# Performance work log

Measured on AMD Instinct MI355X. Metric: run time of the kernel, lower is better.

## Reference

```python
import jax, jax.numpy as jnp
import numpy as np

TOP_K = 8

def setup_inputs() -> dict:
    key = jax.random.key(0)
    kx, kw = jax.random.split(key)
    x = jax.random.normal(kx, (4, 8192, 2048), dtype=jnp.float32)
    # gate weight [n_routed_experts, dim]
    weight = jax.random.normal(kw, (64, 2048), dtype=jnp.float32) * 0.02
    return {"x": x, "weight": weight}

def reference(x, weight):
    # flatten tokens: [N, dim]
    xf = x.reshape(-1, x.shape[-1])
    # router logits: [N, E] = xf @ weight.T
    logits = jnp.einsum('nd,ed->ne', xf, weight)
    scores = jax.nn.softmax(logits, axis=-1)
    # top-k expert scores and indices (lax.top_k returns sorted; torch used
    # sorted=False which is an unordered set of the same elements)
    values, indices = jax.lax.top_k(scores, TOP_K)
    return values, indices
```

## Files before the change

kernel.cpp:

```cpp
#include <hip/hip_runtime.h>
#include <stdint.h>

#define DIM     2048
#define NEXP    64
#define NCHUNK  32
#define TPB     64
#define TAU     5e-5f
#define LCAP    4096

#define WFRAG_USHORTS (NCHUNK * 8192)
#define WT_OFF        (1u << 20)
#define CNT_OFF       (WT_OFF + (1u << 19))
#define LIST_OFF      (CNT_OFF + 16)

typedef __attribute__((ext_vector_type(8))) short bf16x8;
typedef __attribute__((ext_vector_type(8))) unsigned short u16x8;
typedef __attribute__((ext_vector_type(4))) float f32x4;

__device__ inline unsigned short bf16_rne(float f) {
    uint32_t u = __float_as_uint(f);
    return (unsigned short)((u + 0x7FFFu + ((u >> 16) & 1u)) >> 16);
}
__device__ inline float bf16_to_f(unsigned short h) {
    return __uint_as_float(((uint32_t)h) << 16);
}
__device__ inline uint64_t mono64(double d) {
    uint64_t u = (uint64_t)__double_as_longlong(d);
    return (u >> 63) ? ~u : (u | 0x8000000000000000ull);
}
__device__ inline double unmono64(uint64_t m) {
    uint64_t b = (m >> 63) ? (m & 0x7fffffffffffffffull) : ~m;
    return __longlong_as_double((long long)b);
}

#define SPL(F, HV, LV, J)  { unsigned short _h = bf16_rne(F); HV[J] = _h; LV[J] = bf16_rne((F) - bf16_to_f(_h)); }
#define SPLS(F, HV, LV, J) { unsigned short _h = bf16_rne(F); HV[J] = (short)_h; LV[J] = (short)bf16_rne((F) - bf16_to_f(_h)); }

__device__ __forceinline__ void g2l16(const void* g, void* l) {
    __builtin_amdgcn_global_load_lds(
        (__attribute__((address_space(1))) void*)(g),
        (__attribute__((address_space(3))) void*)(l),
        16, 0, 0);
}

__global__ __launch_bounds__(256) void wsplit_kernel(
    const float* __restrict__ wgt, unsigned short* __restrict__ wf)
{
    int g = blockIdx.x * 256 + threadIdx.x;
    int l = g & 63;
    int t = (g >> 6) & 3;
    int s = (g >> 8) & 1;
    int c = g >> 9;
    int e = (l & 15) + 16 * t;
    int k = c * 64 + s * 32 + ((l >> 4) * 8);
    const float* wp = wgt + (size_t)e * DIM + k;
    float4 f0 = *(const float4*)(wp);
    float4 f1 = *(const float4*)(wp + 4);
    u16x8 h, lo;
    SPL(f0.x, h, lo, 0) SPL(f0.y, h, lo, 1) SPL(f0.z, h, lo, 2) SPL(f0.w, h, lo, 3)
    SPL(f1.x, h, lo, 4) SPL(f1.y, h, lo, 5) SPL(f1.z, h, lo, 6) SPL(f1.w, h, lo, 7)
    size_t base = ((((size_t)(c * 2 + s) * 4 + t) * 2 + 0) * 64 + l) * 8;
    *(u16x8*)(wf + base)       = h;
    *(u16x8*)(wf + base + 512) = lo;
}

__global__ __launch_bounds__(256) void wtrans_kernel(
    const float* __restrict__ wgt, float4* __restrict__ wt, int* __restrict__ cnt)
{
    int g  = blockIdx.x * 256 + threadIdx.x;
    if (g == 0) cnt[0] = 0;
    int e  = g >> 9;
    int kq = g & 511;
    float4 v = *(const float4*)(wgt + (size_t)e * DIM + kq * 4);
    wt[(size_t)kq * 64 + e] = v;
}

#define STAGE_CHUNK(CC, XD, BD)                                                   \
    {                                                                             \
        _Pragma("unroll")                                                         \
        for (int s_ = 0; s_ < 4; ++s_) {                                          \
            int idx_ = wave * 256 + s_ * 64 + lane;                               \
            int row_ = idx_ >> 4;                                                 \
            int p_   = idx_ & 15;                                                 \
            int g_   = p_ ^ (row_ & 7);                                           \
            const unsigned char* gsrc_ = (const unsigned char*)x +                \
                (((size_t)(t0 + row_) * DIM + (CC) * 64 + g_ * 4) << 2);          \
            g2l16(gsrc_, (XD) + wave * 4096 + s_ * 1024);                         \
        }                                                                         \
        const unsigned char* wfb_ = (const unsigned char*)wf + (size_t)(CC) * 16384; \
        _Pragma("unroll")                                                         \
        for (int s_ = 0; s_ < 4; ++s_) {                                          \
            g2l16(wfb_ + wave * 4096 + s_ * 1024 + lane * 16,                     \
                  (BD) + wave * 4096 + s_ * 1024);                                \
        }                                                                         \
    }

__global__ __launch_bounds__(256) void moe_gate_mfma_kernel(
    const float* __restrict__ x, const unsigned short* __restrict__ wf,
    float* __restrict__ out, int ntok, int* __restrict__ cnt, int* __restrict__ list)
{
    __shared__ __align__(16) unsigned char smem[65536];

    const int tid  = threadIdx.x;
    const int wave = tid >> 6;
    const int lane = tid & 63;
    const int t0   = blockIdx.x * TPB;
    const int l15  = lane & 15;
    const int lg   = lane >> 4;

    unsigned char* const xb0 = smem;
    unsigned char* const xb1 = smem + 16384;
    unsigned char* const bb0 = smem + 32768;
    unsigned char* const bb1 = smem + 49152;

    f32x4 acc0 = {0.f,0.f,0.f,0.f}, acc1 = {0.f,0.f,0.f,0.f};
    f32x4 acc2 = {0.f,0.f,0.f,0.f}, acc3 = {0.f,0.f,0.f,0.f};

    STAGE_CHUNK(0, xb0, bb0);

    const int s7 = l15 & 7;
    for (int c = 0; c < NCHUNK; ++c) {
        __syncthreads();
        unsigned char* xcur = (c & 1) ? xb1 : xb0;
        unsigned char* bcur = (c & 1) ? bb1 : bb0;
        if (c + 1 < NCHUNK) {
            unsigned char* xnxt = (c & 1) ? xb0 : xb1;
            unsigned char* bnxt = (c & 1) ? bb0 : bb1;
            STAGE_CHUNK(c + 1, xnxt, bnxt);
        }

        const unsigned char* xrow = xcur + (wave * 16 + l15) * 256;
        float4 fa0 = *(const float4*)(xrow + (((2 * lg)     ^ s7) * 16));
        float4 fa1 = *(const float4*)(xrow + (((2 * lg + 1) ^ s7) * 16));
        float4 fa2 = *(const float4*)(xrow + (((8 + 2 * lg) ^ s7) * 16));
        float4 fa3 = *(const float4*)(xrow + (((9 + 2 * lg) ^ s7) * 16));

        bf16x8 Ah0, Al0, Ah1, Al1;
        SPLS(fa0.x, Ah0, Al0, 0) SPLS(fa0.y, Ah0, Al0, 1) SPLS(fa0.z, Ah0, Al0, 2) SPLS(fa0.w, Ah0, Al0, 3)
        SPLS(fa1.x, Ah0, Al0, 4) SPLS(fa1.y, Ah0, Al0, 5) SPLS(fa1.z, Ah0, Al0, 6) SPLS(fa1.w, Ah0, Al0, 7)
        SPLS(fa2.x, Ah1, Al1, 0) SPLS(fa2.y, Ah1, Al1, 1) SPLS(fa2.z, Ah1, Al1, 2) SPLS(fa2.w, Ah1, Al1, 3)
        SPLS(fa3.x, Ah1, Al1, 4) SPLS(fa3.y, Ah1, Al1, 5) SPLS(fa3.z, Ah1, Al1, 6) SPLS(fa3.w, Ah1, Al1, 7)

        const unsigned short* bu = (const unsigned short*)bcur;
        {
            bf16x8 Bh0 = *(const bf16x8*)(bu +        0 + lane * 8);
            bf16x8 Bl0 = *(const bf16x8*)(bu +      512 + lane * 8);
            bf16x8 Bh1 = *(const bf16x8*)(bu + 4096 + 0 + lane * 8);
            bf16x8 Bl1 = *(const bf16x8*)(bu + 4096 + 512 + lane * 8);
            acc0 = __builtin_amdgcn_mfma_f32_16x16x32_bf16(Ah0, Bh0, acc0, 0, 0, 0);
            acc0 = __builtin_amdgcn_mfma_f32_16x16x32_bf16(Ah0, Bl0, acc0, 0, 0, 0);
            acc0 = __builtin_amdgcn_mfma_f32_16x16x32_bf16(Al0, Bh0, acc0, 0, 0, 0);
            acc0 = __builtin_amdgcn_mfma_f32_16x16x32_bf16(Ah1, Bh1, acc0, 0, 0, 0);
            acc0 = __builtin_amdgcn_mfma_f32_16x16x32_bf16(Ah1, Bl1, acc0, 0, 0, 0);
            acc0 = __builtin_amdgcn_mfma_f32_16x16x32_bf16(Al1, Bh1, acc0, 0, 0, 0);
        }
        {
            bf16x8 Bh0 = *(const bf16x8*)(bu + 1024 + lane * 8);
            bf16x8 Bl0 = *(const bf16x8*)(bu + 1536 + lane * 8);
            bf16x8 Bh1 = *(const bf16x8*)(bu + 5120 + lane * 8);
            bf16x8 Bl1 = *(const bf16x8*)(bu + 5632 + lane * 8);
            acc1 = __builtin_amdgcn_mfma_f32_16x16x32_bf16(Ah0, Bh0, acc1, 0, 0, 0);
            acc1 = __builtin_amdgcn_mfma_f32_16x16x32_bf16(Ah0, Bl0, acc1, 0, 0, 0);
            acc1 = __builtin_amdgcn_mfma_f32_16x16x32_bf16(Al0, Bh0, acc1, 0, 0, 0);
            acc1 = __builtin_amdgcn_mfma_f32_16x16x32_bf16(Ah1, Bh1, acc1, 0, 0, 0);
            acc1 = __builtin_amdgcn_mfma_f32_16x16x32_bf16(Ah1, Bl1, acc1, 0, 0, 0);
            acc1 = __builtin_amdgcn_mfma_f32_16x16x32_bf16(Al1, Bh1, acc1, 0, 0, 0);
        }
        {
            bf16x8 Bh0 = *(const bf16x8*)(bu + 2048 + lane * 8);
            bf16x8 Bl0 = *(const bf16x8*)(bu + 2560 + lane * 8);
            bf16x8 Bh1 = *(const bf16x8*)(bu + 6144 + lane * 8);
            bf16x8 Bl1 = *(const bf16x8*)(bu + 6656 + lane * 8);
            acc2 = __builtin_amdgcn_mfma_f32_16x16x32_bf16(Ah0, Bh0, acc2, 0, 0, 0);
            acc2 = __builtin_amdgcn_mfma_f32_16x16x32_bf16(Ah0, Bl0, acc2, 0, 0, 0);
            acc2 = __builtin_amdgcn_mfma_f32_16x16x32_bf16(Al0, Bh0, acc2, 0, 0, 0);
            acc2 = __builtin_amdgcn_mfma_f32_16x16x32_bf16(Ah1, Bh1, acc2, 0, 0, 0);
            acc2 = __builtin_amdgcn_mfma_f32_16x16x32_bf16(Ah1, Bl1, acc2, 0, 0, 0);
            acc2 = __builtin_amdgcn_mfma_f32_16x16x32_bf16(Al1, Bh1, acc2, 0, 0, 0);
        }
        {
            bf16x8 Bh0 = *(const bf16x8*)(bu + 3072 + lane * 8);
            bf16x8 Bl0 = *(const bf16x8*)(bu + 3584 + lane * 8);
            bf16x8 Bh1 = *(const bf16x8*)(bu + 7168 + lane * 8);
            bf16x8 Bl1 = *(const bf16x8*)(bu + 7680 + lane * 8);
            acc3 = __builtin_amdgcn_mfma_f32_16x16x32_bf16(Ah0, Bh0, acc3, 0, 0, 0);
            acc3 = __builtin_amdgcn_mfma_f32_16x16x32_bf16(Ah0, Bl0, acc3, 0, 0, 0);
            acc3 = __builtin_amdgcn_mfma_f32_16x16x32_bf16(Al0, Bh0, acc3, 0, 0, 0);
            acc3 = __builtin_amdgcn_mfma_f32_16x16x32_bf16(Ah1, Bh1, acc3, 0, 0, 0);
            acc3 = __builtin_amdgcn_mfma_f32_16x16x32_bf16(Ah1, Bl1, acc3, 0, 0, 0);
            acc3 = __builtin_amdgcn_mfma_f32_16x16x32_bf16(Al1, Bh1, acc3, 0, 0, 0);
        }
    }

    __syncthreads();
    float* lsw = (float*)smem + wave * 1088;
    {
        const int rb = lg * 4;
        lsw[(rb + 0) * 68 +  0 + l15] = acc0[0]; lsw[(rb + 1) * 68 +  0 + l15] = acc0[1];
        lsw[(rb + 2) * 68 +  0 + l15] = acc0[2]; lsw[(rb + 3) * 68 +  0 + l15] = acc0[3];
        lsw[(rb + 0) * 68 + 16 + l15] = acc1[0]; lsw[(rb + 1) * 68 + 16 + l15] = acc1[1];
        lsw[(rb + 2) * 68 + 16 + l15] = acc1[2]; lsw[(rb + 3) * 68 + 16 + l15] = acc1[3];
        lsw[(rb + 0) * 68 + 32 + l15] = acc2[0]; lsw[(rb + 1) * 68 + 32 + l15] = acc2[1];
        lsw[(rb + 2) * 68 + 32 + l15] = acc2[2]; lsw[(rb + 3) * 68 + 32 + l15] = acc2[3];
        lsw[(rb + 0) * 68 + 48 + l15] = acc3[0]; lsw[(rb + 1) * 68 + 48 + l15] = acc3[1];
        lsw[(rb + 2) * 68 + 48 + l15] = acc3[2]; lsw[(rb + 3) * 68 + 48 + l15] = acc3[3];
    }
    __syncthreads();

    const int tok = l15;
    const int sub = lg;

    float r[16];
#pragma unroll
    for (int k = 0; k < 4; ++k) {
        float4 v = *(const float4*)(&lsw[tok * 68 + sub * 16 + 4 * k]);
        r[4 * k] = v.x; r[4 * k + 1] = v.y; r[4 * k + 2] = v.z; r[4 * k + 3] = v.w;
    }

    float m = r[0];
#pragma unroll
    for (int i = 1; i < 16; ++i) m = fmaxf(m, r[i]);
    m = fmaxf(m, __shfl_xor(m, 16));
    m = fmaxf(m, __shfl_xor(m, 32));

    float ex[16]; float s = 0.f;
#pragma unroll
    for (int i = 0; i < 16; ++i) { ex[i] = expf(r[i] - m); s += ex[i]; }
    s += __shfl_xor(s, 16);
    s += __shfl_xor(s, 32);

    float pr[16];
#pragma unroll
    for (int i = 0; i < 16; ++i) pr[i] = ex[i] / s;

    uint64_t prev = ~0ull;
    float ovals[8]; float oidx[8];
    float prevp = 0.f; int nearf = 0;
#pragma unroll
    for (int p = 0; p < 8; ++p) {
        uint64_t best = 0;
#pragma unroll
        for (int i = 0; i < 16; ++i) {
            uint64_t key = ((uint64_t)__float_as_uint(pr[i]) << 32)
                         | (uint64_t)(63 - (sub * 16 + i));
            if (key < prev && key > best) best = key;
        }
        {
            uint32_t bh = (uint32_t)(best >> 32), bl = (uint32_t)best;
            uint32_t oh = __shfl_xor(bh, 16), ol = __shfl_xor(bl, 16);
            uint64_t ob = ((uint64_t)oh << 32) | ol;
            if (ob > best) best = ob;
            bh = (uint32_t)(best >> 32); bl = (uint32_t)best;
            oh = __shfl_xor(bh, 32); ol = __shfl_xor(bl, 32);
            ob = ((uint64_t)oh << 32) | ol;
            if (ob > best) best = ob;
        }
        prev = best;
        float pv = __uint_as_float((uint32_t)(best >> 32));
        if (p > 0 && (prevp - pv) < TAU * pv) nearf = 1;
        prevp = pv;
        ovals[p] = pv;
        oidx[p]  = (float)(63 - (int)(best & 63));
    }
    {
        uint64_t best = 0;
#pragma unroll
        for (int i = 0; i < 16; ++i) {
            uint64_t key = ((uint64_t)__float_as_uint(pr[i]) << 32)
                         | (uint64_t)(63 - (sub * 16 + i));
            if (key < prev && key > best) best = key;
        }
        {
            uint32_t bh = (uint32_t)(best >> 32), bl = (uint32_t)best;
            uint32_t oh = __shfl_xor(bh, 16), ol = __shfl_xor(bl, 16);
            uint64_t ob = ((uint64_t)oh << 32) | ol;
            if (ob > best) best = ob;
            bh = (uint32_t)(best >> 32); bl = (uint32_t)best;
            oh = __shfl_xor(bh, 32); ol = __shfl_xor(bl, 32);
            ob = ((uint64_t)oh << 32) | ol;
            if (ob > best) best = ob;
        }
        float pv9 = __uint_as_float((uint32_t)(best >> 32));
        if ((prevp - pv9) < TAU * pv9) nearf = 1;
    }

    if (sub == 0) {
        size_t gtok = (size_t)(t0 + wave * 16 + tok);
        float* vo = out + gtok * 8;
        float* io = out + (size_t)ntok * 8 + gtok * 8;
        *(float4*)(vo)     = make_float4(ovals[0], ovals[1], ovals[2], ovals[3]);
        *(float4*)(vo + 4) = make_float4(ovals[4], ovals[5], ovals[6], ovals[7]);
        *(float4*)(io)     = make_float4(oidx[0], oidx[1], oidx[2], oidx[3]);
        *(float4*)(io + 4) = make_float4(oidx[4], oidx[5], oidx[6], oidx[7]);
        if (nearf) {
            int pos = atomicAdd(cnt, 1);
            if (pos < LCAP) list[pos] = (int)gtok;
        }
    }
}

#define QLD(G) \
    float4 wv##G = wq[(size_t)(kq + (G)) * 64 + lane]; \
    float4 xv##G = xq[kq + (G)];
#define QFM(G, A) \
    A = fma((double)xv##G.x, (double)wv##G.x, A); \
    A = fma((double)xv##G.y, (double)wv##G.y, A); \
    A = fma((double)xv##G.z, (double)wv##G.z, A); \
    A = fma((double)xv##G.w, (double)wv##G.w, A);

__global__ __launch_bounds__(256) void moe_gate_refine_kernel(
    const float* __restrict__ x, const float4* __restrict__ wt,
    float* __restrict__ out, int ntok, const int* __restrict__ cnt,
    const int* __restrict__ list)
{
    int c = cnt[0];
    if (c > LCAP) c = LCAP;
    if ((int)blockIdx.x >= c) return;
    const int tok = list[blockIdx.x];

    __shared__ double part[4][64];
    const int wv   = threadIdx.x >> 6;
    const int lane = threadIdx.x & 63;

    const float4* xq = (const float4*)(x + (size_t)tok * DIM) + wv * 128;
    const float4* wq = wt + (size_t)wv * 128 * 64;

    double a0 = 0.0, a1 = 0.0, a2 = 0.0, a3 = 0.0;
    double a4 = 0.0, a5 = 0.0, a6 = 0.0, a7 = 0.0;
#pragma unroll 2
    for (int kq = 0; kq < 128; kq += 8) {
        QLD(0) QLD(1) QLD(2) QLD(3) QLD(4) QLD(5) QLD(6) QLD(7)
        QFM(0, a0) QFM(1, a1) QFM(2, a2) QFM(3, a3)
        QFM(4, a4) QFM(5, a5) QFM(6, a6) QFM(7, a7)
    }
    part[wv][lane] = ((a0 + a1) + (a2 + a3)) + ((a4 + a5) + (a6 + a7));
    __syncthreads();

    if (wv == 0) {
        double acc = (part[0][lane] + part[1][lane]) + (part[2][lane] + part[3][lane]);

        uint64_t mykey = (mono64(acc) & ~63ull) | (uint64_t)(63 - lane);

        uint64_t mk = mykey;
        {
            unsigned long long o;
            o = __shfl_xor((unsigned long long)mk, 1);  if ((uint64_t)o > mk) mk = (uint64_t)o;
            o = __shfl_xor((unsigned long long)mk, 2);  if ((uint64_t)o > mk) mk = (uint64_t)o;
            o = __shfl_xor((unsigned long long)mk, 4);  if ((uint64_t)o > mk) mk = (uint64_t)o;
            o = __shfl_xor((unsigned long long)mk, 8);  if ((uint64_t)o > mk) mk = (uint64_t)o;
            o = __shfl_xor((unsigned long long)mk, 16); if ((uint64_t)o > mk) mk = (uint64_t)o;
            o = __shfl_xor((unsigned long long)mk, 32); if ((uint64_t)o > mk) mk = (uint64_t)o;
        }
        double md = unmono64(mk & ~63ull);

        float s = expf((float)(acc - md));
        s += __shfl_xor(s, 1);
        s += __shfl_xor(s, 2);
        s += __shfl_xor(s, 4);
        s += __shfl_xor(s, 8);
        s += __shfl_xor(s, 16);
        s += __shfl_xor(s, 32);

        float* vo = out + (size_t)tok * 8;
        float* io = out + (size_t)ntok * 8 + (size_t)tok * 8;

        uint64_t prev = ~0ull;
        for (int q = 0; q < 8; ++q) {
            uint64_t best = (mykey < prev) ? mykey : 0;
            {
                unsigned long long o;
                o = __shfl_xor((unsigned long long)best, 1);  if ((uint64_t)o > best) best = (uint64_t)o;
                o = __shfl_xor((unsigned long long)best, 2);  if ((uint64_t)o > best) best = (uint64_t)o;
                o = __shfl_xor((unsigned long long)best, 4);  if ((uint64_t)o > best) best = (uint64_t)o;
                o = __shfl_xor((unsigned long long)best, 8);  if ((uint64_t)o > best) best = (uint64_t)o;
                o = __shfl_xor((unsigned long long)best, 16); if ((uint64_t)o > best) best = (uint64_t)o;
                o = __shfl_xor((unsigned long long)best, 32); if ((uint64_t)o > best) best = (uint64_t)o;
            }
            prev = best;
            if (lane == 0) {
                vo[q] = expf((float)(unmono64(best & ~63ull) - md)) / s;
                io[q] = (float)(63 - (int)(best & 63ull));
            }
        }
    }
}

extern "C" void kernel_launch(void* const* d_in, const int* in_sizes, int n_in,
                              void* d_out, int out_size, void* d_ws, size_t ws_size,
                              hipStream_t stream) {
    const float* x   = (const float*)d_in[0];
    const float* wgt = (const float*)d_in[1];
    float* out = (float*)d_out;
    const int ntok = in_sizes[0] / DIM;

    unsigned short* wf   = (unsigned short*)d_ws;
    float4*         wt   = (float4*)((unsigned char*)d_ws + WT_OFF);
    int*            cnt  = (int*)((unsigned char*)d_ws + CNT_OFF);
    int*            list = (int*)((unsigned char*)d_ws + LIST_OFF);

    hipLaunchKernelGGL(wsplit_kernel, dim3(64), dim3(256), 0, stream, wgt, wf);
    hipLaunchKernelGGL(wtrans_kernel, dim3(128), dim3(256), 0, stream, wgt, wt, cnt);
    hipLaunchKernelGGL(moe_gate_mfma_kernel, dim3(ntok / TPB), dim3(256), 0, stream,
                       x, wf, out, ntok, cnt, list);
    hipLaunchKernelGGL(moe_gate_refine_kernel, dim3(LCAP), dim3(256), 0, stream,
                       x, wt, out, ntok, cnt, list);
}
```

Measured before the change: 90.04 us.

## Read weight fragments directly from global, fuse weight prep kernels, shrink refine grid

Stops staging the pre-split bf16 weight fragments through LDS and has each lane load them straight from global memory (L2/cache resident), halving shared memory per block to allow higher occupancy. The two weight preparation kernels are merged into one launch, and the refine kernel grid cap drops from 4096 to 512 blocks. This trades LDS traffic and a barrier-coupled copy for repeated global/L2 loads per wave, and the smaller list cap risks overflow if many tokens need refinement.

```diff
diff --git a/kernel.cpp b/kernel.cpp
--- a/kernel.cpp
+++ b/kernel.cpp
@@ -6,7 +6,7 @@
 #define NCHUNK  32
 #define TPB     64
 #define TAU     5e-5f
-#define LCAP    4096
+#define LCAP    512
 
 #define WFRAG_USHORTS (NCHUNK * 8192)
 #define WT_OFF        (1u << 20)
@@ -43,39 +43,38 @@
         16, 0, 0);
 }
 
-__global__ __launch_bounds__(256) void wsplit_kernel(
-    const float* __restrict__ wgt, unsigned short* __restrict__ wf)
+__global__ __launch_bounds__(256) void wprep_kernel(
+    const float* __restrict__ wgt, unsigned short* __restrict__ wf,
+    float4* __restrict__ wt, int* __restrict__ cnt)
 {
     int g = blockIdx.x * 256 + threadIdx.x;
-    int l = g & 63;
-    int t = (g >> 6) & 3;
-    int s = (g >> 8) & 1;
-    int c = g >> 9;
-    int e = (l & 15) + 16 * t;
-    int k = c * 64 + s * 32 + ((l >> 4) * 8);
-    const float* wp = wgt + (size_t)e * DIM + k;
-    float4 f0 = *(const float4*)(wp);
-    float4 f1 = *(const float4*)(wp + 4);
-    u16x8 h, lo;
-    SPL(f0.x, h, lo, 0) SPL(f0.y, h, lo, 1) SPL(f0.z, h, lo, 2) SPL(f0.w, h, lo, 3)
-    SPL(f1.x, h, lo, 4) SPL(f1.y, h, lo, 5) SPL(f1.z, h, lo, 6) SPL(f1.w, h, lo, 7)
-    size_t base = ((((size_t)(c * 2 + s) * 4 + t) * 2 + 0) * 64 + l) * 8;
-    *(u16x8*)(wf + base)       = h;
-    *(u16x8*)(wf + base + 512) = lo;
-}
-
-__global__ __launch_bounds__(256) void wtrans_kernel(
-    const float* __restrict__ wgt, float4* __restrict__ wt, int* __restrict__ cnt)
-{
-    int g  = blockIdx.x * 256 + threadIdx.x;
     if (g == 0) cnt[0] = 0;
-    int e  = g >> 9;
-    int kq = g & 511;
-    float4 v = *(const float4*)(wgt + (size_t)e * DIM + kq * 4);
-    wt[(size_t)kq * 64 + e] = v;
-}
-
-#define STAGE_CHUNK(CC, XD, BD)                                                   \
+    {
+        int e  = g >> 9;
+        int kq = g & 511;
+        float4 v = *(const float4*)(wgt + (size_t)e * DIM + kq * 4);
+        wt[(size_t)kq * 64 + e] = v;
+    }
+    if (g < 16384) {
+        int l = g & 63;
+        int t = (g >> 6) & 3;
+        int s = (g >> 8) & 1;
+        int c = g >> 9;
+        int e = (l & 15) + 16 * t;
+        int k = c * 64 + s * 32 + ((l >> 4) * 8);
+        const float* wp = wgt + (size_t)e * DIM + k;
+        float4 f0 = *(const float4*)(wp);
+        float4 f1 = *(const float4*)(wp + 4);
+        u16x8 h, lo;
+        SPL(f0.x, h, lo, 0) SPL(f0.y, h, lo, 1) SPL(f0.z, h, lo, 2) SPL(f0.w, h, lo, 3)
+        SPL(f1.x, h, lo, 4) SPL(f1.y, h, lo, 5) SPL(f1.z, h, lo, 6) SPL(f1.w, h, lo, 7)
+        size_t base = ((((size_t)(c * 2 + s) * 4 + t) * 2 + 0) * 64 + l) * 8;
+        *(u16x8*)(wf + base)       = h;
+        *(u16x8*)(wf + base + 512) = lo;
+    }
+}
+
+#define STAGE_X(CC, XD)                                                           \
     {                                                                             \
         _Pragma("unroll")                                                         \
         for (int s_ = 0; s_ < 4; ++s_) {                                          \
@@ -87,19 +86,13 @@
                 (((size_t)(t0 + row_) * DIM + (CC) * 64 + g_ * 4) << 2);          \
             g2l16(gsrc_, (XD) + wave * 4096 + s_ * 1024);                         \
         }                                                                         \
-        const unsigned char* wfb_ = (const unsigned char*)wf + (size_t)(CC) * 16384; \
-        _Pragma("unroll")                                                         \
-        for (int s_ = 0; s_ < 4; ++s_) {                                          \
-            g2l16(wfb_ + wave * 4096 + s_ * 1024 + lane * 16,                     \
-                  (BD) + wave * 4096 + s_ * 1024);                                \
-        }                                                                         \
     }
 
 __global__ __launch_bounds__(256) void moe_gate_mfma_kernel(
     const float* __restrict__ x, const unsigned short* __restrict__ wf,
     float* __restrict__ out, int ntok, int* __restrict__ cnt, int* __restrict__ list)
 {
-    __shared__ __align__(16) unsigned char smem[65536];
+    __shared__ __align__(16) unsigned char smem[32768];
 
     const int tid  = threadIdx.x;
     const int wave = tid >> 6;
@@ -110,23 +103,20 @@
 
     unsigned char* const xb0 = smem;
     unsigned char* const xb1 = smem + 16384;
-    unsigned char* const bb0 = smem + 32768;
-    unsigned char* const bb1 = smem + 49152;
 
     f32x4 acc0 = {0.f,0.f,0.f,0.f}, acc1 = {0.f,0.f,0.f,0.f};
     f32x4 acc2 = {0.f,0.f,0.f,0.f}, acc3 = {0.f,0.f,0.f,0.f};
 
-    STAGE_CHUNK(0, xb0, bb0);
-
+    STAGE_X(0, xb0);
+
+    const unsigned short* wl = wf + lane * 8;
     const int s7 = l15 & 7;
     for (int c = 0; c < NCHUNK; ++c) {
         __syncthreads();
         unsigned char* xcur = (c & 1) ? xb1 : xb0;
-        unsigned char* bcur = (c & 1) ? bb1 : bb0;
         if (c + 1 < NCHUNK) {
             unsigned char* xnxt = (c & 1) ? xb0 : xb1;
-            unsigned char* bnxt = (c & 1) ? bb0 : bb1;
-            STAGE_CHUNK(c + 1, xnxt, bnxt);
+            STAGE_X(c + 1, xnxt);
         }
 
         const unsigned char* xrow = xcur + (wave * 16 + l15) * 256;
@@ -141,12 +131,12 @@
         SPLS(fa2.x, Ah1, Al1, 0) SPLS(fa2.y, Ah1, Al1, 1) SPLS(fa2.z, Ah1, Al1, 2) SPLS(fa2.w, Ah1, Al1, 3)
         SPLS(fa3.x, Ah1, Al1, 4) SPLS(fa3.y, Ah1, Al1, 5) SPLS(fa3.z, Ah1, Al1, 6) SPLS(fa3.w, Ah1, Al1, 7)
 
-        const unsigned short* bu = (const unsigned short*)bcur;
-        {
-            bf16x8 Bh0 = *(const bf16x8*)(bu +        0 + lane * 8);
-            bf16x8 Bl0 = *(const bf16x8*)(bu +      512 + lane * 8);
-            bf16x8 Bh1 = *(const bf16x8*)(bu + 4096 + 0 + lane * 8);
-            bf16x8 Bl1 = *(const bf16x8*)(bu + 4096 + 512 + lane * 8);
+        const unsigned short* wc = wl + (size_t)c * 8192;
+        {
+            bf16x8 Bh0 = *(const bf16x8*)(wc + 0);
+            bf16x8 Bl0 = *(const bf16x8*)(wc + 512);
+            bf16x8 Bh1 = *(const bf16x8*)(wc + 4096);
+            bf16x8 Bl1 = *(const bf16x8*)(wc + 4608);
             acc0 = __builtin_amdgcn_mfma_f32_16x16x32_bf16(Ah0, Bh0, acc0, 0, 0, 0);
             acc0 = __builtin_amdgcn_mfma_f32_16x16x32_bf16(Ah0, Bl0, acc0, 0, 0, 0);
             acc0 = __builtin_amdgcn_mfma_f32_16x16x32_bf16(Al0, Bh0, acc0, 0, 0, 0);
@@ -155,10 +145,10 @@
             acc0 = __builtin_amdgcn_mfma_f32_16x16x32_bf16(Al1, Bh1, acc0, 0, 0, 0);
         }
         {
-            bf16x8 Bh0 = *(const bf16x8*)(bu + 1024 + lane * 8);
-            bf16x8 Bl0 = *(const bf16x8*)(bu + 1536 + lane * 8);
-            bf16x8 Bh1 = *(const bf16x8*)(bu + 5120 + lane * 8);
-            bf16x8 Bl1 = *(const bf16x8*)(bu + 5632 + lane * 8);
+            bf16x8 Bh0 = *(const bf16x8*)(wc + 1024);
+            bf16x8 Bl0 = *(const bf16x8*)(wc + 1536);
+            bf16x8 Bh1 = *(const bf16x8*)(wc + 5120);
+            bf16x8 Bl1 = *(const bf16x8*)(wc + 5632);
             acc1 = __builtin_amdgcn_mfma_f32_16x16x32_bf16(Ah0, Bh0, acc1, 0, 0, 0);
             acc1 = __builtin_amdgcn_mfma_f32_16x16x32_bf16(Ah0, Bl0, acc1, 0, 0, 0);
             acc1 = __builtin_amdgcn_mfma_f32_16x16x32_bf16(Al0, Bh0, acc1, 0, 0, 0);
@@ -167,10 +157,10 @@
             acc1 = __builtin_amdgcn_mfma_f32_16x16x32_bf16(Al1, Bh1, acc1, 0, 0, 0);
         }
         {
-            bf16x8 Bh0 = *(const bf16x8*)(bu + 2048 + lane * 8);
-            bf16x8 Bl0 = *(const bf16x8*)(bu + 2560 + lane * 8);
-            bf16x8 Bh1 = *(const bf16x8*)(bu + 6144 + lane * 8);
-            bf16x8 Bl1 = *(const bf16x8*)(bu + 6656 + lane * 8);
+            bf16x8 Bh0 = *(const bf16x8*)(wc + 2048);
+            bf16x8 Bl0 = *(const bf16x8*)(wc + 2560);
+            bf16x8 Bh1 = *(const bf16x8*)(wc + 6144);
+            bf16x8 Bl1 = *(const bf16x8*)(wc + 6656);
             acc2 = __builtin_amdgcn_mfma_f32_16x16x32_bf16(Ah0, Bh0, acc2, 0, 0, 0);
             acc2 = __builtin_amdgcn_mfma_f32_16x16x32_bf16(Ah0, Bl0, acc2, 0, 0, 0);
             acc2 = __builtin_amdgcn_mfma_f32_16x16x32_bf16(Al0, Bh0, acc2, 0, 0, 0);
@@ -179,10 +169,10 @@
             acc2 = __builtin_amdgcn_mfma_f32_16x16x32_bf16(Al1, Bh1, acc2, 0, 0, 0);
         }
         {
-            bf16x8 Bh0 = *(const bf16x8*)(bu + 3072 + lane * 8);
-            bf16x8 Bl0 = *(const bf16x8*)(bu + 3584 + lane * 8);
-            bf16x8 Bh1 = *(const bf16x8*)(bu + 7168 + lane * 8);
-            bf16x8 Bl1 = *(const bf16x8*)(bu + 7680 + lane * 8);
+            bf16x8 Bh0 = *(const bf16x8*)(wc + 3072);
+            bf16x8 Bl0 = *(const bf16x8*)(wc + 3584);
+            bf16x8 Bh1 = *(const bf16x8*)(wc + 7168);
+            bf16x8 Bl1 = *(const bf16x8*)(wc + 7680);
             acc3 = __builtin_amdgcn_mfma_f32_16x16x32_bf16(Ah0, Bh0, acc3, 0, 0, 0);
             acc3 = __builtin_amdgcn_mfma_f32_16x16x32_bf16(Ah0, Bl0, acc3, 0, 0, 0);
             acc3 = __builtin_amdgcn_mfma_f32_16x16x32_bf16(Al0, Bh0, acc3, 0, 0, 0);
@@ -398,8 +388,7 @@
     int*            cnt  = (int*)((unsigned char*)d_ws + CNT_OFF);
     int*            list = (int*)((unsigned char*)d_ws + LIST_OFF);
 
-    hipLaunchKernelGGL(wsplit_kernel, dim3(64), dim3(256), 0, stream, wgt, wf);
-    hipLaunchKernelGGL(wtrans_kernel, dim3(128), dim3(256), 0, stream, wgt, wt, cnt);
+    hipLaunchKernelGGL(wprep_kernel, dim3(128), dim3(256), 0, stream, wgt, wf, wt, cnt);
     hipLaunchKernelGGL(moe_gate_mfma_kernel, dim3(ntok / TPB), dim3(256), 0, stream,
                        x, wf, out, ntok, cnt, list);
     hipLaunchKernelGGL(moe_gate_refine_kernel, dim3(LCAP), dim3(256), 0, stream,
```

Measured after the change: 116.9 us. 29.9% more time.
